# Optimization experiments

Hardware: AMD Instinct MI355X
Metric: run time of the kernel (lower is better)

## Reference

```python
import jax, jax.numpy as jnp
import numpy as np

HEADS = 24
HEAD_DIM = 96
SPARSE_N = 4
ROPE_BASE = 10000.0


def _rope_cos_sin(pos, D):
    # pos: [L] int positions; D: per-axis rotary dim (even)
    inv_freq = 1.0 / (ROPE_BASE ** (jnp.arange(0, D, 2, dtype=jnp.float32) / D))
    f = pos.astype(jnp.float32)[:, None] * inv_freq[None, :]   # [L, D/2] (interp scale = 1)
    f = jnp.concatenate([f, f], axis=-1)                        # [L, D]
    return jnp.cos(f), jnp.sin(f)


def _rotate_half(x):
    x1, x2 = jnp.split(x, 2, axis=-1)
    return jnp.concatenate([-x2, x1], axis=-1)


def _apply_rope3d(tok, frame, height, width):
    # tok: [b, h, s, d]; RoPE3D splits head_dim into 3 equal chunks for (t, y, x)
    D = tok.shape[-1] // 3
    t = jnp.repeat(jnp.arange(frame), height * width)
    y = jnp.tile(jnp.repeat(jnp.arange(height), width), frame)
    x = jnp.tile(jnp.arange(width), frame * height)
    outs = []
    for i, pos in enumerate((t, y, x)):
        cos, sin = _rope_cos_sin(pos, D)                        # [s, D]
        part = tok[..., i * D:(i + 1) * D]
        outs.append(part * cos[None, None] + _rotate_half(part) * sin[None, None])
    return jnp.concatenate(outs, axis=-1)


def _sparse_1d(x, n):
    # 'b h (g k) d -> (k b) h g d' with pad so s % n*n == 0
    b, h, s, d = x.shape
    pad = (-s) % (n * n)
    if pad:
        x = jnp.pad(x, ((0, 0), (0, 0), (0, pad), (0, 0)))
    g = (s + pad) // n
    x = x.reshape(b, h, g, n, d)
    return jnp.transpose(x, (3, 0, 1, 2, 4)).reshape(n * b, h, g, d), pad


def _reverse_sparse_1d(x, n, s):
    # '(k b) h g d -> b h (g k) d' then crop to s tokens
    kb, h, g, d = x.shape
    b = kb // n
    x = x.reshape(n, b, h, g, d)
    x = jnp.transpose(x, (1, 2, 3, 0, 4)).reshape(b, h, g * n, d)
    return x[:, :, :s, :]


def setup_inputs() -> dict:
    key = jax.random.key(0)
    ks = jax.random.split(key, 5)
    dim = HEADS * HEAD_DIM
    b, f, hh, ww = 1, 8, 16, 32
    s = f * hh * ww
    inp = {
        "hidden_states": jax.random.normal(ks[0], (b, s, dim), dtype=jnp.float32),
        "wq": jax.random.normal(ks[1], (dim, dim), dtype=jnp.float32) * 0.02,
        "bq": jnp.zeros((dim,), jnp.float32),
        "wk": jax.random.normal(ks[2], (dim, dim), dtype=jnp.float32) * 0.02,
        "bk": jnp.zeros((dim,), jnp.float32),
        "wv": jax.random.normal(ks[3], (dim, dim), dtype=jnp.float32) * 0.02,
        "bv": jnp.zeros((dim,), jnp.float32),
        "wo": jax.random.normal(ks[4], (dim, dim), dtype=jnp.float32) * 0.02,
        "bo": jnp.zeros((dim,), jnp.float32),
        "frame": f, "height": hh, "width": ww,
    }
    return inp


def reference(hidden_states, wq, bq, wk, bk, wv, bv, wo, bo, frame, height, width):
    b, s, dim = hidden_states.shape
    assert s == frame * height * width

    def proj(w, bias):
        y = hidden_states @ w + bias                            # [b, s, dim]
        return jnp.transpose(y.reshape(b, s, HEADS, HEAD_DIM), (0, 2, 1, 3))  # [b, h, s, d]

    q = proj(wq, bq)
    k = proj(wk, bk)
    v = proj(wv, bv)

    # 3D rotary embedding on q, k (self-attention path)
    q = _apply_rope3d(q, frame, height, width)
    k = _apply_rope3d(k, frame, height, width)

    # sparse-1d grouping (sparse_group=False): strided token groups of size s/sparse_n
    q, _ = _sparse_1d(q, SPARSE_N)
    k, _ = _sparse_1d(k, SPARSE_N)
    v, _ = _sparse_1d(v, SPARSE_N)

    scale = 1.0 / jnp.sqrt(jnp.asarray(HEAD_DIM, jnp.float32))
    scores = jnp.einsum('bhqd,bhkd->bhqk', q, k) * scale        # [(n b), h, g, g]
    probs = jax.nn.softmax(scores, axis=-1)
    out = jnp.einsum('bhqk,bhkd->bhqd', probs, v)

    out = _reverse_sparse_1d(out, SPARSE_N, s)                   # [b, h, s, d]
    out = jnp.transpose(out, (0, 2, 1, 3)).reshape(b, s, dim)
    return out @ wo + bo
```

## Files before the change

### kernel.cpp

```cpp
#include <hip/hip_runtime.h>
#include <stdint.h>

#define S_TOK 4096
#define DIM   2304
#define NH    24
#define DH    96
#define GQ    1024
#define KDIM  2304

typedef unsigned short ushort_t;
typedef __attribute__((ext_vector_type(8))) short bf16x8;
typedef __attribute__((ext_vector_type(4))) float f32x4;

__device__ __forceinline__ ushort_t f2bf(float x) {
    union { float f; uint32_t u; } c; c.f = x;
    uint32_t u = c.u + 0x7FFFu + ((c.u >> 16) & 1u);
    return (ushort_t)(u >> 16);
}

#define GLDS(gp, lp) __builtin_amdgcn_global_load_lds( \
    (const __attribute__((address_space(1))) void*)(gp), \
    (__attribute__((address_space(3))) void*)(lp), 16, 0, 0)

__global__ __launch_bounds__(256) void cast_bf16_kernel(const float* __restrict__ in,
                                                        ushort_t* __restrict__ out, int n4) {
    int i = blockIdx.x * 256 + threadIdx.x;
    if (i >= n4) return;
    float4 v = ((const float4*)in)[i];
    ushort4 o;
    o.x = f2bf(v.x); o.y = f2bf(v.y); o.z = f2bf(v.z); o.w = f2bf(v.w);
    ((ushort4*)out)[i] = o;
}

__global__ __launch_bounds__(256) void wtrans_kernel(const float* __restrict__ W0,
                                                     const float* __restrict__ W1,
                                                     const float* __restrict__ W2,
                                                     const float* __restrict__ W3,
                                                     ushort_t* __restrict__ WT0, int dim) {
    __shared__ float tile[32][33];
    const int z = blockIdx.z;
    const float* W = (z == 0) ? W0 : (z == 1) ? W1 : (z == 2) ? W2 : W3;
    ushort_t* WT = WT0 + (size_t)z * dim * dim;
    const int bx = blockIdx.x * 32;
    const int by = blockIdx.y * 32;
    const int tx = threadIdx.x & 31, ty = threadIdx.x >> 5;
#pragma unroll
    for (int i = 0; i < 4; ++i)
        tile[ty + i*8][tx] = W[(size_t)(by + ty + i*8) * dim + bx + tx];
    __syncthreads();
#pragma unroll
    for (int i = 0; i < 4; ++i)
        WT[(size_t)(bx + ty + i*8) * dim + by + tx] = f2bf(tile[tx][ty + i*8]);
}

template<bool FINAL>
__global__ __launch_bounds__(512, 2) void gemm256(const ushort_t* __restrict__ A,
                                                  const ushort_t* __restrict__ Bt,
                                                  const float* __restrict__ bq,
                                                  const float* __restrict__ bk,
                                                  const float* __restrict__ bv,
                                                  ushort_t* __restrict__ Qb,
                                                  ushort_t* __restrict__ Kb,
                                                  ushort_t* __restrict__ Vtb,
                                                  float* __restrict__ Cf) {
    constexpr int K  = KDIM;
    constexpr int NT = K / 32;
    __shared__ ushort_t a_s[4 * 8192];
    __shared__ ushort_t b_s[4 * 8192];
    const int t = threadIdx.x, l = t & 63, w = t >> 6;
    const int wr = w >> 2, wc = w & 3, g = l >> 4, ln = l & 15;
    const int nwg = gridDim.x * gridDim.y;
    const int lin = blockIdx.y * gridDim.x + blockIdx.x;
    const int cpx = nwg >> 3;
    const int swz = (lin & 7) * cpx + (lin >> 3);
    const int bx = swz % gridDim.x, by = swz / gridDim.x;
    const int m0 = by * 256, n0 = bx * 256;

    const int swz_rd = (g ^ ((ln >> 1) & 3)) * 8;
    const int kc_src = (((t & 3) ^ ((t >> 3) & 3)) * 8);
    const int srow   = t >> 2;

    auto stageA = [&](int kt) {
        const int slot = kt & 3;
#pragma unroll
        for (int q = 0; q < 2; ++q)
            GLDS(A + (size_t)(m0 + q*128 + srow) * K + kt*32 + kc_src,
                 &a_s[slot*8192 + (q*512 + t) * 8]);
    };
    auto stageB = [&](int kt) {
        const int slot = kt & 3;
#pragma unroll
        for (int q = 0; q < 2; ++q)
            GLDS(Bt + (size_t)(n0 + q*128 + srow) * K + kt*32 + kc_src,
                 &b_s[slot*8192 + (q*512 + t) * 8]);
    };

    f32x4 acc[8][4] = {};

    stageA(0); stageB(0); stageA(1); stageB(1); stageA(2); stageB(2);
    asm volatile("s_waitcnt vmcnt(8)" ::: "memory");
    __builtin_amdgcn_s_barrier();

    for (int kt = 0; kt < NT; ++kt) {
        const int slot = kt & 3;
        bf16x8 bv4[4];
        {
            bf16x8 av[4];
#pragma unroll
            for (int j = 0; j < 4; ++j)
                bv4[j] = *(const bf16x8*)&b_s[slot*8192 + (wc*64 + j*16 + ln)*32 + swz_rd];
#pragma unroll
            for (int i = 0; i < 4; ++i)
                av[i] = *(const bf16x8*)&a_s[slot*8192 + (wr*128 + i*16 + ln)*32 + swz_rd];
            if (kt < NT - 3) stageA(kt + 3);
            __builtin_amdgcn_s_barrier();
            asm volatile("s_waitcnt lgkmcnt(0)" ::: "memory");
            __builtin_amdgcn_sched_barrier(0);
            __builtin_amdgcn_s_setprio(1);
#pragma unroll
            for (int i = 0; i < 4; ++i)
#pragma unroll
                for (int j = 0; j < 4; ++j)
                    acc[i][j] = __builtin_amdgcn_mfma_f32_16x16x32_bf16(av[i], bv4[j], acc[i][j], 0, 0, 0);
            __builtin_amdgcn_s_setprio(0);
        }
        {
            bf16x8 av[4];
#pragma unroll
            for (int i = 0; i < 4; ++i)
                av[i] = *(const bf16x8*)&a_s[slot*8192 + (wr*128 + 64 + i*16 + ln)*32 + swz_rd];
            if (kt < NT - 3) stageB(kt + 3);
            if (kt <= NT - 4)      asm volatile("s_waitcnt vmcnt(8)" ::: "memory");
            else if (kt == NT - 3) asm volatile("s_waitcnt vmcnt(4)" ::: "memory");
            else                   asm volatile("s_waitcnt vmcnt(0)" ::: "memory");
            __builtin_amdgcn_s_barrier();
            asm volatile("s_waitcnt lgkmcnt(0)" ::: "memory");
            __builtin_amdgcn_sched_barrier(0);
            __builtin_amdgcn_s_setprio(1);
#pragma unroll
            for (int i = 0; i < 4; ++i)
#pragma unroll
                for (int j = 0; j < 4; ++j)
                    acc[4 + i][j] = __builtin_amdgcn_mfma_f32_16x16x32_bf16(av[i], bv4[j], acc[4 + i][j], 0, 0, 0);
            __builtin_amdgcn_s_setprio(0);
        }
    }

    if constexpr (FINAL) {
        const float* bias = bq;
#pragma unroll
        for (int i = 0; i < 8; ++i) {
            int mb = m0 + wr*128 + i*16 + g*4;
#pragma unroll
            for (int j = 0; j < 4; ++j) {
                int n = n0 + wc*64 + j*16 + ln;
                float bb = bias[n];
#pragma unroll
                for (int r = 0; r < 4; ++r)
                    Cf[(size_t)(mb + r) * DIM + n] = acc[i][j][r] + bb;
            }
        }
    } else {
        const int mode = bx / 9;
        const int nb = (bx - mode * 9) * 256;
        const float* bias = (mode == 0) ? bq : (mode == 1) ? bk : bv;
        if (mode == 2) {
#pragma unroll
            for (int i = 0; i < 8; ++i) {
                int mb = m0 + wr*128 + i*16 + g*4;
                int q  = mb >> 2;
#pragma unroll
                for (int j = 0; j < 4; ++j) {
                    int nm = nb + wc*64 + j*16 + ln;
                    int hh = nm / DH, d = nm - hh * DH;
                    float bb = bias[nm];
#pragma unroll
                    for (int r = 0; r < 4; ++r)
                        Vtb[(size_t)(r * NH + hh) * (DH * GQ) + (size_t)d * GQ + q] =
                            f2bf(acc[i][j][r] + bb);
                }
            }
        } else {
            ushort_t* O = (mode == 0) ? Qb : Kb;
            const float scq = (mode == 0) ? 0.1020620726159658f : 1.0f;
#pragma unroll
            for (int i = 0; i < 8; ++i) {
                int mb = m0 + wr*128 + i*16 + g*4;
#pragma unroll
                for (int jp = 0; jp < 2; ++jp) {
                    int j  = jp * 2;
                    int n1 = nb + wc*64 + j*16 + ln;
                    int hh = n1 / DH, d1 = n1 - hh * DH;
                    int sec = d1 >> 5, f = d1 & 15;
                    float invf = __expf((float)f * -0.5756462732485114f);
                    float b1 = bias[n1], b2 = bias[n1 + 16];
#pragma unroll
                    for (int r = 0; r < 4; ++r) {
                        int m = mb + r;
                        int pos = (sec == 0) ? (m >> 9) : (sec == 1) ? ((m >> 5) & 15) : (m & 31);
                        float ang = (float)pos * invf;
                        float sn, cs;
                        __sincosf(ang, &sn, &cs);
                        float v1 = acc[i][j][r]     + b1;
                        float v2 = acc[i][j + 1][r] + b2;
                        size_t base = ((size_t)((m & 3) * NH + hh)) * (GQ * DH) + (size_t)(m >> 2) * DH;
                        O[base + d1]      = f2bf((v1 * cs - v2 * sn) * scq);
                        O[base + d1 + 16] = f2bf((v2 * cs + v1 * sn) * scq);
                    }
                }
            }
        }
    }
}

__global__ __launch_bounds__(256, 3) void attn_kernel(const ushort_t* __restrict__ Qb,
                                                      const ushort_t* __restrict__ Kb,
                                                      const ushort_t* __restrict__ Vt,
                                                      ushort_t* __restrict__ ATT) {
    __shared__ ushort_t k_s[2][12 * 64 * 8];
    __shared__ ushort_t v_s[8 * 96 * 8];
    __shared__ ushort_t p_s[4 * 2 * 16 * 64];

    const int t = threadIdx.x, l = t & 63, w = t >> 6, g = l >> 4, ln = l & 15;
    const int lin  = blockIdx.x;
    const int swz  = (lin & 7) * 96 + (lin >> 3);
    const int inst = swz >> 3;
    const int qb0  = (swz & 7) * 128;
    const int n_idx = inst / NH, h = inst - n_idx * NH;
    const int swzp = (ln & 7) << 3;

    const ushort_t* Qi = Qb + (size_t)inst * (GQ * DH);
    const ushort_t* Ki = Kb + (size_t)inst * (GQ * DH);
    const ushort_t* Vi = Vt + (size_t)inst * (DH * GQ);

    auto stageK = [&](int kt, int b) {
#pragma unroll
        for (int it = 0; it < 3; ++it) {
            int P = t + it * 256;
            int c = P >> 6, key = P & 63;
            GLDS(Ki + (size_t)(kt * 64 + key) * DH + c * 8, &k_s[b][P * 8]);
        }
    };
    auto stageV = [&](int kt) {
#pragma unroll
        for (int it = 0; it < 3; ++it) {
            int P = t + it * 256;
            int c = P / 96, d = P - c * 96;
            GLDS(Vi + (size_t)d * GQ + kt * 64 + c * 8, &v_s[P * 8]);
        }
    };

    bf16x8 qf[2][3];
#pragma unroll
    for (int qt = 0; qt < 2; ++qt)
#pragma unroll
        for (int ks = 0; ks < 3; ++ks)
            qf[qt][ks] = *(const bf16x8*)(Qi + (size_t)(qb0 + w*32 + qt*16 + ln) * DH + ks*32 + g*8);

    float m_run[2], l_run[2];
#pragma unroll
    for (int qt = 0; qt < 2; ++qt) { m_run[qt] = -3.0e38f; l_run[qt] = 0.f; }
    f32x4 acc_o[2][6] = {};

    stageK(0, 0);
    stageV(0);
    __syncthreads();

    int cur = 0;
    for (int kt = 0; kt < 16; ++kt) {
        stageK((kt + 1) & 15, cur ^ 1);
        float al2[2];

        f32x4 sc[2][4] = {};
#pragma unroll
        for (int ct = 0; ct < 4; ++ct) {
            bf16x8 kf0 = *(const bf16x8*)&k_s[cur][((0*4 + g)*64 + ct*16 + ln) * 8];
            bf16x8 kf1 = *(const bf16x8*)&k_s[cur][((1*4 + g)*64 + ct*16 + ln) * 8];
            bf16x8 kf2 = *(const bf16x8*)&k_s[cur][((2*4 + g)*64 + ct*16 + ln) * 8];
#pragma unroll
            for (int qi = 0; qi < 2; ++qi) {
                sc[qi][ct] = __builtin_amdgcn_mfma_f32_16x16x32_bf16(kf0, qf[qi][0], sc[qi][ct], 0, 0, 0);
                sc[qi][ct] = __builtin_amdgcn_mfma_f32_16x16x32_bf16(kf1, qf[qi][1], sc[qi][ct], 0, 0, 0);
                sc[qi][ct] = __builtin_amdgcn_mfma_f32_16x16x32_bf16(kf2, qf[qi][2], sc[qi][ct], 0, 0, 0);
            }
        }
#pragma unroll
        for (int qi = 0; qi < 2; ++qi) {
            const int qt = qi;
            float mx = sc[qi][0][0];
#pragma unroll
            for (int ct = 0; ct < 4; ++ct)
#pragma unroll
                for (int r = 0; r < 4; ++r)
                    mx = fmaxf(mx, sc[qi][ct][r]);
            mx = fmaxf(mx, __shfl_xor(mx, 16, 64));
            mx = fmaxf(mx, __shfl_xor(mx, 32, 64));
            float mn = fmaxf(m_run[qt], mx);
            float al = __expf(m_run[qt] - mn);
            m_run[qt] = mn;
            float rs = 0.f;
            ushort_t pb[16];
#pragma unroll
            for (int ct = 0; ct < 4; ++ct)
#pragma unroll
                for (int r = 0; r < 4; ++r) {
                    float p = __expf(sc[qi][ct][r] - mn);
                    rs += p;
                    pb[ct*4 + r] = f2bf(p);
                }
            rs += __shfl_xor(rs, 16, 64);
            rs += __shfl_xor(rs, 32, 64);
            l_run[qt] = l_run[qt] * al + rs;
            al2[qt] = al;
            const int pbase = ((w*2 + qt)*16 + ln) * 64;
#pragma unroll
            for (int ct = 0; ct < 4; ++ct) {
                ushort4 pk;
                pk.x = pb[ct*4+0]; pk.y = pb[ct*4+1]; pk.z = pb[ct*4+2]; pk.w = pb[ct*4+3];
                *(ushort4*)&p_s[pbase + ((ct*16 + g*4) ^ swzp)] = pk;
            }
        }

#pragma unroll
        for (int qt = 0; qt < 2; ++qt)
#pragma unroll
            for (int r = 0; r < 4; ++r) {
                float a = __shfl(al2[qt], g*4 + r, 16);
#pragma unroll
                for (int dt = 0; dt < 6; ++dt)
                    acc_o[qt][dt][r] *= a;
            }

        asm volatile("s_waitcnt vmcnt(3)" ::: "memory");
        __builtin_amdgcn_s_barrier();
        __builtin_amdgcn_sched_barrier(0);
        asm volatile("s_waitcnt lgkmcnt(0)" ::: "memory");
        __builtin_amdgcn_sched_barrier(0);

#pragma unroll
        for (int kb = 0; kb < 2; ++kb) {
            bf16x8 pf2[2];
#pragma unroll
            for (int qt = 0; qt < 2; ++qt)
                pf2[qt] = *(const bf16x8*)&p_s[((w*2 + qt)*16 + ln)*64 + ((kb*32 + g*8) ^ swzp)];
#pragma unroll
            for (int dt = 0; dt < 6; ++dt) {
                bf16x8 vf = *(const bf16x8*)&v_s[((kb*4 + g)*96 + dt*16 + ln) * 8];
#pragma unroll
                for (int qt = 0; qt < 2; ++qt)
                    acc_o[qt][dt] = __builtin_amdgcn_mfma_f32_16x16x32_bf16(pf2[qt], vf, acc_o[qt][dt], 0, 0, 0);
            }
        }

        __syncthreads();
        if (kt < 15) stageV(kt + 1);
        cur ^= 1;
    }

#pragma unroll
    for (int qt = 0; qt < 2; ++qt) {
        float inv = 1.0f / l_run[qt];
#pragma unroll
        for (int r = 0; r < 4; ++r) {
            float iv = __shfl(inv, g*4 + r, 16);
            int gq = qb0 + w*32 + qt*16 + g*4 + r;
            size_t base = ((size_t)(gq * 4 + n_idx)) * DIM + h * DH;
#pragma unroll
            for (int dt = 0; dt < 6; ++dt)
                ATT[base + dt*16 + ln] = f2bf(acc_o[qt][dt][r] * iv);
        }
    }
}

extern "C" void kernel_launch(void* const* d_in, const int* in_sizes, int n_in,
                              void* d_out, int out_size, void* d_ws, size_t ws_size,
                              hipStream_t stream) {
    const float* hidden = (const float*)d_in[0];
    const float* wq = (const float*)d_in[1];
    const float* bq = (const float*)d_in[2];
    const float* wk = (const float*)d_in[3];
    const float* bk = (const float*)d_in[4];
    const float* wv = (const float*)d_in[5];
    const float* bv = (const float*)d_in[6];
    const float* wo = (const float*)d_in[7];
    const float* bo = (const float*)d_in[8];
    float* out = (float*)d_out;

    char* ws = (char*)d_ws;
    ushort_t* Xb  = (ushort_t*)ws;
    ushort_t* WTq = (ushort_t*)(ws + 18874368);
    ushort_t* WTk = WTq + (size_t)DIM * DIM;
    ushort_t* WTv = WTk + (size_t)DIM * DIM;
    ushort_t* WTo = WTv + (size_t)DIM * DIM;
    ushort_t* Qb  = WTo + (size_t)DIM * DIM;
    ushort_t* Kb  = Qb + (size_t)S_TOK * DIM;
    ushort_t* Vtb = Kb + (size_t)S_TOK * DIM;
    ushort_t* ATT = Vtb + (size_t)S_TOK * DIM;

    cast_bf16_kernel<<<dim3(9216), dim3(256), 0, stream>>>(hidden, Xb, (S_TOK * DIM) / 4);

    wtrans_kernel<<<dim3(72, 72, 4), 256, 0, stream>>>(wq, wk, wv, wo, WTq, DIM);

    gemm256<false><<<dim3(27, 16), 512, 0, stream>>>(Xb, WTq, bq, bk, bv, Qb, Kb, Vtb, nullptr);

    attn_kernel<<<dim3(768), 256, 0, stream>>>(Qb, Kb, Vtb, ATT);

    gemm256<true><<<dim3(9, 16), 512, 0, stream>>>(ATT, WTo, bo, nullptr, nullptr,
                                                   nullptr, nullptr, nullptr, out);
}
```

Before: 332.4 us.

## Deepen GEMM LDS ring to five stages with one barrier per k-step

The bf16 GEMM shared-memory ring grows from four to five slots. Loads now prefetch four k-tiles ahead, and A and B for tile kt+4 are issued together after the MFMAs. The per-k-step structure drops from two barriers to one. The next tile's B fragments are loaded into registers while the current tile's MFMAs run, with partial lgkmcnt waits so LDS reads overlap compute. LDS use rises to 160 KB per block, which keeps occupancy at one block per CU and adds register pressure from the extra prefetch buffers.

```diff
diff --git a/kernel.cpp b/kernel.cpp
--- a/kernel.cpp
+++ b/kernel.cpp
@@ -65,8 +65,8 @@
                                                   float* __restrict__ Cf) {
     constexpr int K  = KDIM;
     constexpr int NT = K / 32;
-    __shared__ ushort_t a_s[4 * 8192];
-    __shared__ ushort_t b_s[4 * 8192];
+    __shared__ ushort_t a_s[5 * 8192];
+    __shared__ ushort_t b_s[5 * 8192];
     const int t = threadIdx.x, l = t & 63, w = t >> 6;
     const int wr = w >> 2, wc = w & 3, g = l >> 4, ln = l & 15;
     const int nwg = gridDim.x * gridDim.y;
@@ -81,14 +81,14 @@
     const int srow   = t >> 2;
 
     auto stageA = [&](int kt) {
-        const int slot = kt & 3;
+        const int slot = kt % 5;
 #pragma unroll
         for (int q = 0; q < 2; ++q)
             GLDS(A + (size_t)(m0 + q*128 + srow) * K + kt*32 + kc_src,
                  &a_s[slot*8192 + (q*512 + t) * 8]);
     };
     auto stageB = [&](int kt) {
-        const int slot = kt & 3;
+        const int slot = kt % 5;
 #pragma unroll
         for (int q = 0; q < 2; ++q)
             GLDS(Bt + (size_t)(n0 + q*128 + srow) * K + kt*32 + kc_src,
@@ -97,53 +97,59 @@
 
     f32x4 acc[8][4] = {};
 
-    stageA(0); stageB(0); stageA(1); stageB(1); stageA(2); stageB(2);
+    stageA(0); stageB(0); stageA(1); stageB(1);
+    stageA(2); stageB(2); stageA(3); stageB(3);
     asm volatile("s_waitcnt vmcnt(8)" ::: "memory");
     __builtin_amdgcn_s_barrier();
 
+    bf16x8 bv_cur[4], bv_nxt[4];
+#pragma unroll
+    for (int j = 0; j < 4; ++j)
+        bv_cur[j] = *(const bf16x8*)&b_s[(wc*64 + j*16 + ln)*32 + swz_rd];
+
     for (int kt = 0; kt < NT; ++kt) {
-        const int slot = kt & 3;
-        bf16x8 bv4[4];
-        {
-            bf16x8 av[4];
+        const int sA = (kt % 5) * 8192;
+        const int sB = ((kt + 1) % 5) * 8192;
+        bf16x8 av0[4], av1[4];
+#pragma unroll
+        for (int i = 0; i < 4; ++i)
+            av0[i] = *(const bf16x8*)&a_s[sA + (wr*128 + i*16 + ln)*32 + swz_rd];
+#pragma unroll
+        for (int i = 0; i < 4; ++i)
+            av1[i] = *(const bf16x8*)&a_s[sA + (wr*128 + 64 + i*16 + ln)*32 + swz_rd];
+#pragma unroll
+        for (int j = 0; j < 4; ++j)
+            bv_nxt[j] = *(const bf16x8*)&b_s[sB + (wc*64 + j*16 + ln)*32 + swz_rd];
+
+        asm volatile("s_waitcnt lgkmcnt(8)" ::: "memory");
+        __builtin_amdgcn_sched_barrier(0);
+        __builtin_amdgcn_s_setprio(1);
+#pragma unroll
+        for (int i = 0; i < 4; ++i)
 #pragma unroll
             for (int j = 0; j < 4; ++j)
-                bv4[j] = *(const bf16x8*)&b_s[slot*8192 + (wc*64 + j*16 + ln)*32 + swz_rd];
-#pragma unroll
-            for (int i = 0; i < 4; ++i)
-                av[i] = *(const bf16x8*)&a_s[slot*8192 + (wr*128 + i*16 + ln)*32 + swz_rd];
-            if (kt < NT - 3) stageA(kt + 3);
-            __builtin_amdgcn_s_barrier();
-            asm volatile("s_waitcnt lgkmcnt(0)" ::: "memory");
-            __builtin_amdgcn_sched_barrier(0);
-            __builtin_amdgcn_s_setprio(1);
-#pragma unroll
-            for (int i = 0; i < 4; ++i)
-#pragma unroll
-                for (int j = 0; j < 4; ++j)
-                    acc[i][j] = __builtin_amdgcn_mfma_f32_16x16x32_bf16(av[i], bv4[j], acc[i][j], 0, 0, 0);
-            __builtin_amdgcn_s_setprio(0);
-        }
-        {
-            bf16x8 av[4];
-#pragma unroll
-            for (int i = 0; i < 4; ++i)
-                av[i] = *(const bf16x8*)&a_s[slot*8192 + (wr*128 + 64 + i*16 + ln)*32 + swz_rd];
-            if (kt < NT - 3) stageB(kt + 3);
-            if (kt <= NT - 4)      asm volatile("s_waitcnt vmcnt(8)" ::: "memory");
-            else if (kt == NT - 3) asm volatile("s_waitcnt vmcnt(4)" ::: "memory");
-            else                   asm volatile("s_waitcnt vmcnt(0)" ::: "memory");
-            __builtin_amdgcn_s_barrier();
-            asm volatile("s_waitcnt lgkmcnt(0)" ::: "memory");
-            __builtin_amdgcn_sched_barrier(0);
-            __builtin_amdgcn_s_setprio(1);
-#pragma unroll
-            for (int i = 0; i < 4; ++i)
-#pragma unroll
-                for (int j = 0; j < 4; ++j)
-                    acc[4 + i][j] = __builtin_amdgcn_mfma_f32_16x16x32_bf16(av[i], bv4[j], acc[4 + i][j], 0, 0, 0);
-            __builtin_amdgcn_s_setprio(0);
-        }
+                acc[i][j] = __builtin_amdgcn_mfma_f32_16x16x32_bf16(av0[i], bv_cur[j], acc[i][j], 0, 0, 0);
+        __builtin_amdgcn_s_setprio(0);
+
+        asm volatile("s_waitcnt lgkmcnt(4)" ::: "memory");
+        __builtin_amdgcn_sched_barrier(0);
+        __builtin_amdgcn_s_setprio(1);
+#pragma unroll
+        for (int i = 0; i < 4; ++i)
+#pragma unroll
+            for (int j = 0; j < 4; ++j)
+                acc[4 + i][j] = __builtin_amdgcn_mfma_f32_16x16x32_bf16(av1[i], bv_cur[j], acc[4 + i][j], 0, 0, 0);
+        __builtin_amdgcn_s_setprio(0);
+
+        if (kt + 4 < NT) { stageA(kt + 4); stageB(kt + 4); }
+        if (kt <= NT - 5)      asm volatile("s_waitcnt vmcnt(8)" ::: "memory");
+        else if (kt == NT - 4) asm volatile("s_waitcnt vmcnt(4)" ::: "memory");
+        else if (kt == NT - 3) asm volatile("s_waitcnt vmcnt(0)" ::: "memory");
+        asm volatile("s_waitcnt lgkmcnt(0)" ::: "memory");
+        __builtin_amdgcn_sched_barrier(0);
+        __builtin_amdgcn_s_barrier();
+#pragma unroll
+        for (int j = 0; j < 4; ++j) bv_cur[j] = bv_nxt[j];
     }
 
     if constexpr (FINAL) {
```

New measurement: 335.5 us. Within noise of the previous version (+0.9%).
